# Kernel tuning notes

Measured on AMD Instinct MI355X. Metric: run time of the kernel, lower is better.

The kernel has to match this reference:

```python
import jax, jax.numpy as jnp
import numpy as np

N = 20000
E = 320000
F_IN = 512
F_OUT = 512
DIFF_T = 1.0
NUM_STEPS = 5
TIME_DECAY = 0.1
LN_EPS = 1e-5


def setup_inputs() -> dict:
    key = jax.random.key(0)
    k_x, k_e, k_ts, k_wt, k_wr = jax.random.split(key, 5)
    x = jax.random.normal(k_x, (N, F_IN), dtype=jnp.float32)
    edge_index = jax.random.randint(k_e, (2, E), 0, N)
    timestamps = jax.random.uniform(k_ts, (E,), dtype=jnp.float32) * 100.0
    lim = float(np.sqrt(6.0 / (F_IN + F_OUT)))  # xavier_uniform
    W_t = jax.random.uniform(k_wt, (F_OUT, F_IN), jnp.float32, -lim, lim)
    b_t = jnp.zeros((F_OUT,), jnp.float32)
    W_r = jax.random.uniform(k_wr, (F_OUT, F_IN), jnp.float32, -lim, lim)
    gamma = jnp.ones((F_OUT,), jnp.float32)
    beta = jnp.zeros((F_OUT,), jnp.float32)
    return {"node_features": x, "edge_index": edge_index, "timestamps": timestamps,
            "W_t": W_t, "b_t": b_t, "W_r": W_r, "gamma": gamma, "beta": beta,
            "graph_time": 100}


def reference(node_features, edge_index, timestamps, W_t, b_t, W_r, gamma, beta, graph_time):
    x = node_features
    n = x.shape[0]
    # append self-loops with timestamp == graph.time
    loop = jnp.arange(n)
    ei = jnp.concatenate([edge_index, jnp.stack([loop, loop], axis=0)], axis=1)
    ts = jnp.concatenate([timestamps, jnp.full((n,), graph_time, jnp.float32)])
    src, dst = ei[0], ei[1]
    # time-decayed symmetric-normalized adjacency weights
    w = jnp.exp(-TIME_DECAY * (ts.max() - ts))  # [E+N]
    deg = jax.ops.segment_sum(w, dst, num_segments=n)  # [N]
    dinv = jnp.where(deg > 0, deg ** -0.5, 0.0)
    ew = dinv[src] * w * dinv[dst]  # [E+N]
    # K Euler steps of heat diffusion: h <- h + dt*(A_norm h - h)
    dt = DIFF_T / NUM_STEPS
    h = x
    for _ in range(NUM_STEPS):
        diffused = jax.ops.segment_sum(ew[:, None] * h[src], dst, num_segments=n)  # [N, F]
        h = h + dt * (diffused - h)
    # transform + residual + layernorm (dropout omitted: eval mode)
    out = jax.nn.relu(h @ W_t.T + b_t) + x @ W_r.T  # [N, F_OUT]
    mu = out.mean(axis=-1, keepdims=True)
    var = out.var(axis=-1, keepdims=True)
    out = (out - mu) * jax.lax.rsqrt(var + LN_EPS) * gamma + beta
    return out
```

## Files before the change

### kernel.cpp

```cpp
#include <hip/hip_runtime.h>
#include <hip/hip_fp16.h>

#define FDIM 512
#define TDK  0.1f
#define DTs  0.2f
#define EPSv 1e-5f

using bf16x8  = __attribute__((ext_vector_type(8))) __bf16;
using floatx4 = __attribute__((ext_vector_type(4))) float;
using ushort8 = __attribute__((ext_vector_type(8))) unsigned short;
using uintx4  = __attribute__((ext_vector_type(4))) unsigned int;

__device__ __forceinline__ unsigned short f2bf(float f) {
  unsigned int u = __float_as_uint(f);
  u += 0x7fffu + ((u >> 16) & 1u);
  return (unsigned short)(u >> 16);
}

__device__ __forceinline__ void gld16(const __bf16* g, __bf16* l) {
  __builtin_amdgcn_global_load_lds(
      (const __attribute__((address_space(1))) unsigned int*)g,
      (__attribute__((address_space(3))) unsigned int*)l, 16, 0, 0);
}

__global__ __launch_bounds__(256) void edge_w_deg(const int* __restrict__ src, const int* __restrict__ dst,
                                                  const float* __restrict__ ts, const int* __restrict__ gt_p,
                                                  float* __restrict__ w, unsigned long long* __restrict__ pc,
                                                  int E, int N) {
  int e = blockIdx.x * blockDim.x + threadIdx.x;
  int total = E + N;
  if (e >= total) return;
  float gtf = (float)(*gt_p);
  int d; float t;
  if (e < E) { d = dst[e]; t = ts[e]; }
  else       { d = e - E;  t = gtf; }
  float wv = expf(TDK * (t - gtf));
  w[e] = wv;
  unsigned long long pk = (1ULL << 52) + (unsigned long long)(wv * 4294967296.0f);
  atomicAdd(&pc[d], pk);
}

__global__ __launch_bounds__(256) void seg_reduce(const unsigned long long* __restrict__ pc,
                                                  int* __restrict__ bsum, int n) {
  int i = blockIdx.x * 256 + threadIdx.x;
  int v = (i < n) ? (int)(pc[i] >> 52) : 0;
  for (int o = 32; o; o >>= 1) v += __shfl_down(v, o);
  __shared__ int sm[4];
  if ((threadIdx.x & 63) == 0) sm[threadIdx.x >> 6] = v;
  __syncthreads();
  if (threadIdx.x == 0) bsum[blockIdx.x] = sm[0] + sm[1] + sm[2] + sm[3];
}

__global__ __launch_bounds__(256) void scan_bsum(const int* __restrict__ bsum, int* __restrict__ bbase, int nb) {
  __shared__ int sm[256];
  int t = threadIdx.x;
  int v = (t < nb) ? bsum[t] : 0;
  sm[t] = v;
  __syncthreads();
  for (int o = 1; o < 256; o <<= 1) {
    int u = (t >= o) ? sm[t - o] : 0;
    __syncthreads();
    sm[t] += u;
    __syncthreads();
  }
  if (t < nb) bbase[t] = sm[t] - v;
}

__global__ __launch_bounds__(256) void seg_scan(const unsigned long long* __restrict__ pc,
                                                const int* __restrict__ bbase,
                                                int* __restrict__ offs, int* __restrict__ cursor,
                                                float* __restrict__ dinv, int n, int totE) {
  __shared__ int sm[256];
  int i = blockIdx.x * 256 + threadIdx.x;
  unsigned long long p = (i < n) ? pc[i] : 0ULL;
  int v = (int)(p >> 52);
  sm[threadIdx.x] = v;
  __syncthreads();
  for (int o = 1; o < 256; o <<= 1) {
    int u = (threadIdx.x >= o) ? sm[threadIdx.x - o] : 0;
    __syncthreads();
    sm[threadIdx.x] += u;
    __syncthreads();
  }
  int excl = sm[threadIdx.x] - v + bbase[blockIdx.x];
  if (i < n) {
    offs[i] = excl; cursor[i] = excl;
    float deg = (float)(p & ((1ULL << 52) - 1ULL)) * (1.0f / 4294967296.0f);
    dinv[i] = (deg > 0.f) ? rsqrtf(deg) : 0.f;
  }
  if (i == 0) offs[n] = totE;
}

__global__ __launch_bounds__(256) void scatter_kernel(const int* __restrict__ src, const int* __restrict__ dst,
                                                      const float* __restrict__ w, const float* __restrict__ dinv,
                                                      int* __restrict__ cursor, unsigned* __restrict__ cv,
                                                      int E, int N) {
  int e = blockIdx.x * blockDim.x + threadIdx.x;
  if (e >= E + N) return;
  int s, d;
  if (e < E) { s = src[e]; d = dst[e]; }
  else       { s = d = e - E; }
  int pos = atomicAdd(&cursor[d], 1);
  float v = dinv[s] * w[e] * dinv[d];
  unsigned short hv = __half_as_ushort(__float2half(v));
  cv[pos] = (unsigned)s | ((unsigned)hv << 16);
}

__device__ __forceinline__ void acc8(uintx4 u, float v, float* a) {
  a[0] += v * __uint_as_float(u[0] << 16);
  a[1] += v * __uint_as_float(u[0] & 0xffff0000u);
  a[2] += v * __uint_as_float(u[1] << 16);
  a[3] += v * __uint_as_float(u[1] & 0xffff0000u);
  a[4] += v * __uint_as_float(u[2] << 16);
  a[5] += v * __uint_as_float(u[2] & 0xffff0000u);
  a[6] += v * __uint_as_float(u[3] << 16);
  a[7] += v * __uint_as_float(u[3] & 0xffff0000u);
}

__device__ __forceinline__ float cvval(unsigned cu) {
  return __half2float(__ushort_as_half((unsigned short)(cu >> 16)));
}

__global__ __launch_bounds__(256) void spmm_xcd(const int* __restrict__ offs, const unsigned* __restrict__ cv,
                                                const unsigned short* __restrict__ h_in,
                                                unsigned short* __restrict__ h_out, int N) {
  int chunk = blockIdx.x & 7;
  int tile  = blockIdx.x >> 3;
  int row = tile * 32 + (threadIdx.x >> 3);
  if (row >= N) return;
  int fo = chunk * 64 + (threadIdx.x & 7) * 8;
  const unsigned short* hp = h_in + fo;
  int s = offs[row], e = offs[row + 1];
  float a[8] = {0.f, 0.f, 0.f, 0.f, 0.f, 0.f, 0.f, 0.f};
  int j = s;
  for (; j + 8 <= e; j += 8) {
    unsigned cu[8]; uintx4 u[8];
#pragma unroll
    for (int t = 0; t < 8; ++t) cu[t] = cv[j + t];
#pragma unroll
    for (int t = 0; t < 8; ++t) u[t] = *(const uintx4*)(hp + ((cu[t] & 0xffffu) << 9));
#pragma unroll
    for (int t = 0; t < 8; ++t) acc8(u[t], cvval(cu[t]), a);
  }
  if (j + 4 <= e) {
    unsigned cu[4]; uintx4 u[4];
#pragma unroll
    for (int t = 0; t < 4; ++t) cu[t] = cv[j + t];
#pragma unroll
    for (int t = 0; t < 4; ++t) u[t] = *(const uintx4*)(hp + ((cu[t] & 0xffffu) << 9));
#pragma unroll
    for (int t = 0; t < 4; ++t) acc8(u[t], cvval(cu[t]), a);
    j += 4;
  }
  for (; j < e; ++j) {
    unsigned cu = cv[j];
    uintx4 u = *(const uintx4*)(hp + ((cu & 0xffffu) << 9));
    acc8(u, cvval(cu), a);
  }
  uintx4 ud = *(const uintx4*)(hp + (row << 9));
  float hd[8];
  hd[0] = __uint_as_float(ud[0] << 16); hd[1] = __uint_as_float(ud[0] & 0xffff0000u);
  hd[2] = __uint_as_float(ud[1] << 16); hd[3] = __uint_as_float(ud[1] & 0xffff0000u);
  hd[4] = __uint_as_float(ud[2] << 16); hd[5] = __uint_as_float(ud[2] & 0xffff0000u);
  hd[6] = __uint_as_float(ud[3] << 16); hd[7] = __uint_as_float(ud[3] & 0xffff0000u);
  uintx4 o;
  unsigned int p0, p1;
#define PACK(k0, k1, dst_)                                        \
  { float o0 = hd[k0] + DTs * (a[k0] - hd[k0]);                   \
    float o1 = hd[k1] + DTs * (a[k1] - hd[k1]);                   \
    p0 = f2bf(o0); p1 = f2bf(o1); dst_ = p0 | (p1 << 16); }
  PACK(0, 1, o[0]) PACK(2, 3, o[1]) PACK(4, 5, o[2]) PACK(6, 7, o[3])
#undef PACK
  __builtin_nontemporal_store(o, (uintx4*)(h_out + (size_t)row * FDIM + fo));
}

__global__ __launch_bounds__(256) void cast_all(const float* __restrict__ x, const float* __restrict__ wt,
                                                const float* __restrict__ wr,
                                                unsigned short* __restrict__ xb, unsigned short* __restrict__ wtb,
                                                unsigned short* __restrict__ wrb, int n8x, int n8w) {
  int i = blockIdx.x * blockDim.x + threadIdx.x;
  const float* sp; unsigned short* dp; int k;
  if (i < n8x)                { sp = x;  dp = xb;  k = i; }
  else if (i < n8x + n8w)     { sp = wt; dp = wtb; k = i - n8x; }
  else if (i < n8x + 2 * n8w) { sp = wr; dp = wrb; k = i - n8x - n8w; }
  else return;
  const float4 v0 = *(const float4*)(sp + (size_t)k * 8);
  const float4 v1 = *(const float4*)(sp + (size_t)k * 8 + 4);
  ushort8 o;
  o[0] = f2bf(v0.x); o[1] = f2bf(v0.y); o[2] = f2bf(v0.z); o[3] = f2bf(v0.w);
  o[4] = f2bf(v1.x); o[5] = f2bf(v1.y); o[6] = f2bf(v1.z); o[7] = f2bf(v1.w);
  *(ushort8*)(dp + (size_t)k * 8) = o;
}

__global__ __launch_bounds__(256, 3) void gemm_fused(const __bf16* __restrict__ Ah, const __bf16* __restrict__ Ax,
                                                     const __bf16* __restrict__ Wt, const __bf16* __restrict__ Wr,
                                                     const float* __restrict__ bias, float* __restrict__ out,
                                                     int M, int NB) {
  __shared__ __bf16 sA[2][128 * 32];
  __shared__ __bf16 sB[2][128 * 32];
  int tid = threadIdx.x;
  int wid = tid >> 6, lane = tid & 63;
  int wm = wid & 1, wn = wid >> 1;
  int lane15 = lane & 15, quad = lane >> 4;

  int d = blockIdx.x;
  int x = d & 7, s = d >> 3;
  int q = NB >> 3, r = NB & 7;
  int g = (x < r ? x * (q + 1) : r * (q + 1) + (x - r) * q) + s;
  int mi = g >> 2, ni = g & 3;
  int m0 = mi * 128, n0 = ni * 128;

  int r0 = wid * 32 + (lane >> 2);
  int c0 = ((((lane & 3) - (lane >> 3)) & 3)) * 8;
  int am0 = m0 + r0;      if (am0 >= M) am0 = M - 1;
  int am1 = m0 + r0 + 16; if (am1 >= M) am1 = M - 1;
  int bn0 = n0 + r0;
  const __bf16* a00 = Ah + (size_t)am0 * FDIM + c0;
  const __bf16* a01 = Ah + (size_t)am1 * FDIM + c0;
  const __bf16* a10 = Ax + (size_t)am0 * FDIM + c0;
  const __bf16* a11 = Ax + (size_t)am1 * FDIM + c0;
  const __bf16* b00 = Wt + (size_t)bn0 * FDIM + c0;
  const __bf16* b01 = Wt + (size_t)(bn0 + 16) * FDIM + c0;
  const __bf16* b10 = Wr + (size_t)bn0 * FDIM + c0;
  const __bf16* b11 = Wr + (size_t)(bn0 + 16) * FDIM + c0;
  int loff0 = wid * 1024;
  int loff1 = wid * 1024 + 512;

  auto stage = [&](int b, const __bf16* pa0, const __bf16* pa1,
                   const __bf16* pb0, const __bf16* pb1, int kt) {
    gld16(pa0 + kt, &sA[b][loff0]); gld16(pa1 + kt, &sA[b][loff1]);
    gld16(pb0 + kt, &sB[b][loff0]); gld16(pb1 + kt, &sB[b][loff1]);
  };

  int koff = ((quad + (lane15 >> 1)) & 3) * 8;

  float bn[4];
#pragma unroll
  for (int in = 0; in < 4; ++in) bn[in] = bias[n0 + wn * 64 + in * 16 + lane15];

  floatx4 acc[4][4];
  floatx4 z4; z4[0] = 0.f; z4[1] = 0.f; z4[2] = 0.f; z4[3] = 0.f;
#pragma unroll
  for (int im = 0; im < 4; ++im)
#pragma unroll
    for (int in = 0; in < 4; ++in) acc[im][in] = z4;

  stage(0, a00, a01, b00, b01, 0);
  for (int it = 0; it < 32; ++it) {
    int cb = it & 1;
    __syncthreads();
    int nx = it + 1;
    if (nx < 32) {
      if (nx < 16) stage(1 - cb, a00, a01, b00, b01, nx * 32);
      else         stage(1 - cb, a10, a11, b10, b11, (nx & 15) * 32);
    }
    if (it == 16) {
#pragma unroll
      for (int im = 0; im < 4; ++im)
#pragma unroll
        for (int in = 0; in < 4; ++in)
#pragma unroll
          for (int rr = 0; rr < 4; ++rr)
            acc[im][in][rr] = fmaxf(acc[im][in][rr] + bn[in], 0.f);
    }
    bf16x8 af[4], br[4];
#pragma unroll
    for (int im = 0; im < 4; ++im)
      af[im] = *(const bf16x8*)(&sA[cb][(wm * 64 + im * 16 + lane15) * 32 + koff]);
#pragma unroll
    for (int in = 0; in < 4; ++in)
      br[in] = *(const bf16x8*)(&sB[cb][(wn * 64 + in * 16 + lane15) * 32 + koff]);
#pragma unroll
    for (int im = 0; im < 4; ++im)
#pragma unroll
      for (int in = 0; in < 4; ++in)
        acc[im][in] = __builtin_amdgcn_mfma_f32_16x16x32_bf16(af[im], br[in], acc[im][in], 0, 0, 0);
  }

#pragma unroll
  for (int im = 0; im < 4; ++im) {
#pragma unroll
    for (int in = 0; in < 4; ++in) {
#pragma unroll
      for (int rr = 0; rr < 4; ++rr) {
        int m = m0 + wm * 64 + im * 16 + quad * 4 + rr;
        int n = n0 + wn * 64 + in * 16 + lane15;
        if (m < M) out[(size_t)m * FDIM + n] = acc[im][in][rr];
      }
    }
  }
}

__global__ __launch_bounds__(256) void ln_kernel(const float* __restrict__ pre, const float* __restrict__ gamma,
                                                 const float* __restrict__ beta, float* __restrict__ out) {
  int row = blockIdx.x, t = threadIdx.x;
  float2 v = *(const float2*)(pre + (size_t)row * FDIM + t * 2);
  float s = v.x + v.y;
  float ss = v.x * v.x + v.y * v.y;
  for (int off = 32; off; off >>= 1) { s += __shfl_down(s, off); ss += __shfl_down(ss, off); }
  __shared__ float sm[4], sm2[4];
  int wid = t >> 6, lane = t & 63;
  if (lane == 0) { sm[wid] = s; sm2[wid] = ss; }
  __syncthreads();
  if (t == 0) {
    float a = sm[0] + sm[1] + sm[2] + sm[3];
    float b = sm2[0] + sm2[1] + sm2[2] + sm2[3];
    sm[0] = a; sm2[0] = b;
  }
  __syncthreads();
  float mu = sm[0] * (1.f / FDIM);
  float var = sm2[0] * (1.f / FDIM) - mu * mu;
  float inv = rsqrtf(var + EPSv);
  float2 g  = *(const float2*)(gamma + t * 2);
  float2 bb = *(const float2*)(beta + t * 2);
  float2 o;
  o.x = (v.x - mu) * inv * g.x + bb.x;
  o.y = (v.y - mu) * inv * g.y + bb.y;
  *(float2*)(out + (size_t)row * FDIM + t * 2) = o;
}

extern "C" void kernel_launch(void* const* d_in, const int* in_sizes, int n_in,
                              void* d_out, int out_size, void* d_ws, size_t ws_size,
                              hipStream_t stream) {
  const float* x     = (const float*)d_in[0];
  const int*   ei    = (const int*)d_in[1];
  const float* ts    = (const float*)d_in[2];
  const float* W_t   = (const float*)d_in[3];
  const float* b_t   = (const float*)d_in[4];
  const float* W_r   = (const float*)d_in[5];
  const float* gamma = (const float*)d_in[6];
  const float* beta  = (const float*)d_in[7];
  const int*   gt    = (const int*)d_in[8];

  const int E = in_sizes[2];
  const int N = in_sizes[0] / FDIM;
  const int* src = ei;
  const int* dst = ei + E;
  const int totE = E + N;
  const int nb = (N + 255) / 256;

  char* base = (char*)d_ws;
  size_t off = 0;
  auto carve = [&](size_t bytes) -> char* {
    char* r = base + off;
    off = (off + bytes + 255) & ~(size_t)255;
    return r;
  };
  unsigned long long* pc = (unsigned long long*)carve((size_t)N * 8);
  size_t zero_bytes = off;
  float* dinv  = (float*)carve((size_t)N * 4);
  int*   offs  = (int*)  carve((size_t)(N + 1) * 4);
  int*   cursor= (int*)  carve((size_t)N * 4);
  int*   bsum  = (int*)  carve((size_t)nb * 4);
  int*   bbase = (int*)  carve((size_t)nb * 4);
  float* w     = (float*)carve((size_t)totE * 4);
  unsigned* cv = (unsigned*)carve((size_t)totE * 4);
  unsigned short* xb  = (unsigned short*)carve((size_t)N * FDIM * 2);
  unsigned short* hba = (unsigned short*)carve((size_t)N * FDIM * 2);
  unsigned short* hbb = (unsigned short*)carve((size_t)N * FDIM * 2);
  unsigned short* wtb = (unsigned short*)carve((size_t)FDIM * FDIM * 2);
  unsigned short* wrb = (unsigned short*)carve((size_t)FDIM * FDIM * 2);
  float* preLN = (float*)carve((size_t)N * FDIM * 4);

  hipMemsetAsync(d_ws, 0, zero_bytes, stream);

  edge_w_deg<<<(totE + 255) / 256, 256, 0, stream>>>(src, dst, ts, gt, w, pc, E, N);
  seg_reduce<<<nb, 256, 0, stream>>>(pc, bsum, N);
  scan_bsum<<<1, 256, 0, stream>>>(bsum, bbase, nb);
  seg_scan<<<nb, 256, 0, stream>>>(pc, bbase, offs, cursor, dinv, N, totE);
  scatter_kernel<<<(totE + 255) / 256, 256, 0, stream>>>(src, dst, w, dinv, cursor, cv, E, N);

  int n8x = N * FDIM / 8;
  int n8w = FDIM * FDIM / 8;
  int n8tot = n8x + 2 * n8w;
  cast_all<<<(n8tot + 255) / 256, 256, 0, stream>>>(x, W_t, W_r, xb, wtb, wrb, n8x, n8w);

  int sgrid = ((N + 31) / 32) * 8;
  spmm_xcd<<<sgrid, 256, 0, stream>>>(offs, cv, xb,  hba, N);
  spmm_xcd<<<sgrid, 256, 0, stream>>>(offs, cv, hba, hbb, N);
  spmm_xcd<<<sgrid, 256, 0, stream>>>(offs, cv, hbb, hba, N);
  spmm_xcd<<<sgrid, 256, 0, stream>>>(offs, cv, hba, hbb, N);
  spmm_xcd<<<sgrid, 256, 0, stream>>>(offs, cv, hbb, hba, N);

  int MB = (N + 127) / 128;
  int NBLK = MB * (FDIM / 128);
  gemm_fused<<<NBLK, 256, 0, stream>>>((const __bf16*)hba, (const __bf16*)xb,
                                       (const __bf16*)wtb, (const __bf16*)wrb,
                                       b_t, preLN, N, NBLK);

  ln_kernel<<<N, 256, 0, stream>>>(preLN, gamma, beta, (float*)d_out);
}
```

Baseline: 354.1 us.

## Split each row's edges across eight lane groups per wavefront in SpMM

The SpMM kernel now assigns one wavefront per row per 64-feature chunk. Eight 8-lane groups each take every eighth edge and combine their partial sums with a cross-lane shuffle reduction. Before, each 8-thread group walked all of a row's edges serially with deep per-thread unrolling. The aim is more parallel gathers in flight and less load imbalance from long rows, in exchange for eight times more blocks, shuffle overhead and only one group in eight storing results.

Result: slower. 491.5 us (+38.8%).

```diff
diff --git a/kernel.cpp b/kernel.cpp
--- a/kernel.cpp
+++ b/kernel.cpp
@@ -124,54 +124,64 @@
 __global__ __launch_bounds__(256) void spmm_xcd(const int* __restrict__ offs, const unsigned* __restrict__ cv,
                                                 const unsigned short* __restrict__ h_in,
                                                 unsigned short* __restrict__ h_out, int N) {
-  int chunk = blockIdx.x & 7;
-  int tile  = blockIdx.x >> 3;
-  int row = tile * 32 + (threadIdx.x >> 3);
+  int chunk  = blockIdx.x & 7;
+  int rowblk = blockIdx.x >> 3;
+  int wid = threadIdx.x >> 6, lane = threadIdx.x & 63;
+  int row = rowblk * 4 + wid;
   if (row >= N) return;
-  int fo = chunk * 64 + (threadIdx.x & 7) * 8;
+  int es = lane >> 3;
+  int l7 = lane & 7;
+  int fo = chunk * 64 + l7 * 8;
   const unsigned short* hp = h_in + fo;
   int s = offs[row], e = offs[row + 1];
   float a[8] = {0.f, 0.f, 0.f, 0.f, 0.f, 0.f, 0.f, 0.f};
   int j = s;
-  for (; j + 8 <= e; j += 8) {
-    unsigned cu[8]; uintx4 u[8];
-#pragma unroll
-    for (int t = 0; t < 8; ++t) cu[t] = cv[j + t];
-#pragma unroll
-    for (int t = 0; t < 8; ++t) u[t] = *(const uintx4*)(hp + ((cu[t] & 0xffffu) << 9));
-#pragma unroll
-    for (int t = 0; t < 8; ++t) acc8(u[t], cvval(cu[t]), a);
-  }
-  if (j + 4 <= e) {
-    unsigned cu[4]; uintx4 u[4];
-#pragma unroll
-    for (int t = 0; t < 4; ++t) cu[t] = cv[j + t];
-#pragma unroll
-    for (int t = 0; t < 4; ++t) u[t] = *(const uintx4*)(hp + ((cu[t] & 0xffffu) << 9));
-#pragma unroll
-    for (int t = 0; t < 4; ++t) acc8(u[t], cvval(cu[t]), a);
-    j += 4;
-  }
-  for (; j < e; ++j) {
-    unsigned cu = cv[j];
-    uintx4 u = *(const uintx4*)(hp + ((cu & 0xffffu) << 9));
-    acc8(u, cvval(cu), a);
-  }
-  uintx4 ud = *(const uintx4*)(hp + (row << 9));
-  float hd[8];
-  hd[0] = __uint_as_float(ud[0] << 16); hd[1] = __uint_as_float(ud[0] & 0xffff0000u);
-  hd[2] = __uint_as_float(ud[1] << 16); hd[3] = __uint_as_float(ud[1] & 0xffff0000u);
-  hd[4] = __uint_as_float(ud[2] << 16); hd[5] = __uint_as_float(ud[2] & 0xffff0000u);
-  hd[6] = __uint_as_float(ud[3] << 16); hd[7] = __uint_as_float(ud[3] & 0xffff0000u);
-  uintx4 o;
-  unsigned int p0, p1;
+  for (; j + 16 <= e; j += 16) {
+    unsigned c0 = cv[j + es];
+    unsigned c1 = cv[j + 8 + es];
+    uintx4 u0 = *(const uintx4*)(hp + ((c0 & 0xffffu) << 9));
+    uintx4 u1 = *(const uintx4*)(hp + ((c1 & 0xffffu) << 9));
+    acc8(u0, cvval(c0), a);
+    acc8(u1, cvval(c1), a);
+  }
+  if (j + 8 <= e) {
+    unsigned c0 = cv[j + es];
+    uintx4 u0 = *(const uintx4*)(hp + ((c0 & 0xffffu) << 9));
+    acc8(u0, cvval(c0), a);
+    j += 8;
+  }
+  if (j < e) {
+    int idx = j + es;
+    unsigned c0 = 0;
+    uintx4 u0; u0[0] = 0; u0[1] = 0; u0[2] = 0; u0[3] = 0;
+    if (idx < e) {
+      c0 = cv[idx];
+      u0 = *(const uintx4*)(hp + ((c0 & 0xffffu) << 9));
+    }
+    acc8(u0, cvval(c0), a);
+  }
+#pragma unroll
+  for (int o = 8; o <= 32; o <<= 1) {
+#pragma unroll
+    for (int k = 0; k < 8; ++k) a[k] += __shfl_xor(a[k], o);
+  }
+  if (es == 0) {
+    uintx4 ud = *(const uintx4*)(hp + (row << 9));
+    float hd[8];
+    hd[0] = __uint_as_float(ud[0] << 16); hd[1] = __uint_as_float(ud[0] & 0xffff0000u);
+    hd[2] = __uint_as_float(ud[1] << 16); hd[3] = __uint_as_float(ud[1] & 0xffff0000u);
+    hd[4] = __uint_as_float(ud[2] << 16); hd[5] = __uint_as_float(ud[2] & 0xffff0000u);
+    hd[6] = __uint_as_float(ud[3] << 16); hd[7] = __uint_as_float(ud[3] & 0xffff0000u);
+    uintx4 o;
+    unsigned int p0, p1;
 #define PACK(k0, k1, dst_)                                        \
-  { float o0 = hd[k0] + DTs * (a[k0] - hd[k0]);                   \
-    float o1 = hd[k1] + DTs * (a[k1] - hd[k1]);                   \
-    p0 = f2bf(o0); p1 = f2bf(o1); dst_ = p0 | (p1 << 16); }
-  PACK(0, 1, o[0]) PACK(2, 3, o[1]) PACK(4, 5, o[2]) PACK(6, 7, o[3])
+    { float o0 = hd[k0] + DTs * (a[k0] - hd[k0]);                 \
+      float o1 = hd[k1] + DTs * (a[k1] - hd[k1]);                 \
+      p0 = f2bf(o0); p1 = f2bf(o1); dst_ = p0 | (p1 << 16); }
+    PACK(0, 1, o[0]) PACK(2, 3, o[1]) PACK(4, 5, o[2]) PACK(6, 7, o[3])
 #undef PACK
-  __builtin_nontemporal_store(o, (uintx4*)(h_out + (size_t)row * FDIM + fo));
+    __builtin_nontemporal_store(o, (uintx4*)(h_out + (size_t)row * FDIM + fo));
+  }
 }
 
 __global__ __launch_bounds__(256) void cast_all(const float* __restrict__ x, const float* __restrict__ wt,
@@ -375,7 +385,7 @@
   int n8tot = n8x + 2 * n8w;
   cast_all<<<(n8tot + 255) / 256, 256, 0, stream>>>(x, W_t, W_r, xb, wtb, wrb, n8x, n8w);
 
-  int sgrid = ((N + 31) / 32) * 8;
+  int sgrid = ((N + 3) / 4) * 8;
   spmm_xcd<<<sgrid, 256, 0, stream>>>(offs, cv, xb,  hba, N);
   spmm_xcd<<<sgrid, 256, 0, stream>>>(offs, cv, hba, hbb, N);
   spmm_xcd<<<sgrid, 256, 0, stream>>>(offs, cv, hbb, hba, N);
```
